# Kernel tuning notes

Measured on AMD Instinct MI355X. Metric: run time of the kernel, lower is better.

## Reference

```python
import jax, jax.numpy as jnp
import numpy as np

NUM_HEADS = 16


def setup_inputs() -> dict:
    key = jax.random.key(0)
    ks = jax.random.split(key, 6)
    B, S, E = 2, 2048, 1024
    scale = 1.0 / np.sqrt(E)
    return {
        "x": jax.random.normal(ks[0], (B, S, E), dtype=jnp.float32),
        "mask": jnp.ones((B, S), dtype=jnp.int32),
        "Wq": jax.random.normal(ks[1], (E, E), dtype=jnp.float32) * scale,
        "bq": jnp.zeros((E,), dtype=jnp.float32),
        "Wk": jax.random.normal(ks[2], (E, E), dtype=jnp.float32) * scale,
        "bk": jnp.zeros((E,), dtype=jnp.float32),
        "Wv": jax.random.normal(ks[3], (E, E), dtype=jnp.float32) * scale,
        "bv": jnp.zeros((E,), dtype=jnp.float32),
        "Wo": jax.random.normal(ks[4], (E, E), dtype=jnp.float32) * scale,
        "bo": jnp.zeros((E,), dtype=jnp.float32),
    }


def reference(x, mask, Wq, bq, Wk, bk, Wv, bv, Wo, bo):
    B, S, E = x.shape
    H = NUM_HEADS
    D = E // H

    def heads(t):  # [B,S,E] -> [B,H,S,D]
        return t.reshape(B, S, H, D).transpose(0, 2, 1, 3)

    q = heads(x @ Wq + bq)
    k = heads(x @ Wk + bk)
    v = heads(x @ Wv + bv)

    # scaled dot-product scores [B,H,S,S]
    scores = jnp.einsum("bhsd,bhtd->bhst", q, k) / jnp.sqrt(jnp.float32(D))
    m = mask.astype(jnp.float32)[:, None, None, :]  # key-side padding mask
    scores = scores + (-1e9) * (1.0 - m)
    weights = jax.nn.softmax(scores, axis=-1)
    attn = jnp.einsum("bhst,bhtd->bhsd", weights, v)

    concat = attn.transpose(0, 2, 1, 3).reshape(B, S, E)
    return concat @ Wo + bo
```

## Files before the change

kernel.cpp:

```cpp
#include <hip/hip_runtime.h>
#include <stdint.h>

#define E_DIM   1024
#define HNUM    16
#define DH      64
#define BATCH   2
#define SEQ     2048
#define M_TOT   (BATCH*SEQ)
#define LOG2E   1.44269504088896340736f

typedef __bf16 bf16x8 __attribute__((ext_vector_type(8)));
typedef __bf16 bf16x4 __attribute__((ext_vector_type(4)));
typedef float  f32x4  __attribute__((ext_vector_type(4)));
typedef float  f32x16 __attribute__((ext_vector_type(16)));
typedef unsigned short u16;
typedef unsigned int   u32;
typedef unsigned long long u64;
typedef u16 u16x8 __attribute__((ext_vector_type(8)));
typedef u32 u32x2 __attribute__((ext_vector_type(2)));
typedef u32 u32x4 __attribute__((ext_vector_type(4)));

__device__ __forceinline__ u16 f2bf(float f) {
    u32 u = __builtin_bit_cast(u32, f);
    u32 r = 0x7FFFu + ((u >> 16) & 1u);
    return (u16)((u + r) >> 16);
}

__device__ __forceinline__ void gload_lds16(const u16* g, u16* l) {
    __builtin_amdgcn_global_load_lds(
        (const __attribute__((address_space(1))) u32*)g,
        (__attribute__((address_space(3))) u32*)l, 16, 0, 0);
}

__device__ __forceinline__ u32 cvt_pk_bf16(float lo, float hi) {
    u32 r;
    asm("v_cvt_pk_bf16_f32 %0, %1, %2" : "=v"(r) : "v"(lo), "v"(hi));
    return r;
}

#define MFMA16(a,b,c) __builtin_amdgcn_mfma_f32_16x16x32_bf16((a),(b),(c),0,0,0)
#define MFMA32(a,b,c) __builtin_amdgcn_mfma_f32_32x32x16_bf16((a),(b),(c),0,0,0)

__global__ __launch_bounds__(256) void prep_kernel(
    const float* __restrict__ x, u16* __restrict__ out,
    const int* __restrict__ mask, u64* __restrict__ bits,
    const float* __restrict__ w0, const float* __restrict__ w1,
    const float* __restrict__ w2, const float* __restrict__ w3,
    u16* __restrict__ wt) {
    __shared__ float tile[32][33];
    const int bid = blockIdx.x;
    const int tid = threadIdx.x;
    if (bid < M_TOT * E_DIM / 1024) {
        const int idx = (bid * 256 + tid) * 4;
        float4 v = *reinterpret_cast<const float4*>(x + idx);
        ushort4 o;
        o.x = f2bf(v.x); o.y = f2bf(v.y); o.z = f2bf(v.z); o.w = f2bf(v.w);
        *reinterpret_cast<ushort4*>(out + idx) = o;
        if (bid < M_TOT / 256) {
            const int i = bid * 256 + tid;
            u64 bl = __ballot(mask[i] != 0);
            if ((i & 63) == 0) bits[i >> 6] = bl;
        }
    } else {
        const int wb = bid - M_TOT * E_DIM / 1024;
        const int z = wb >> 10;
        const int rem = wb & 1023;
        const int n0 = (rem & 31) * 32, k0 = (rem >> 5) * 32;
        const int tx = tid & 31, ty = tid >> 5;
        const float* w = z == 0 ? w0 : z == 1 ? w1 : z == 2 ? w2 : w3;
        #pragma unroll
        for (int j = 0; j < 4; j++) {
            int k = k0 + ty + j * 8;
            tile[ty + j * 8][tx] = w[(size_t)k * E_DIM + n0 + tx];
        }
        __syncthreads();
        u16* o = wt + (size_t)z * E_DIM * E_DIM;
        #pragma unroll
        for (int j = 0; j < 4; j++) {
            int n = n0 + ty + j * 8;
            o[(size_t)n * E_DIM + k0 + tx] = f2bf(tile[tx][ty + j * 8]);
        }
    }
}

template <typename OutT>
__global__ __launch_bounds__(256) void gemm_kernel(
    const u16* __restrict__ A, const u16* __restrict__ Bt_base, OutT* __restrict__ C_base,
    const float* __restrict__ bias0, const float* __restrict__ bias1,
    const float* __restrict__ bias2, float scale0, int Mdim) {
    const int z = blockIdx.z;
    const u16* Bt = Bt_base + (size_t)z * E_DIM * E_DIM;
    OutT* C = C_base + (size_t)z * Mdim * E_DIM;
    const float* bias = (z == 0) ? bias0 : (z == 1 ? bias1 : bias2);
    const float scale = (z == 0) ? scale0 : 1.0f;

    __shared__ __align__(16) u16 Als[128 * 32];
    __shared__ __align__(16) u16 Bls[128 * 32];

    const int tid = threadIdx.x;
    const int lane = tid & 63;
    const int w = tid >> 6;
    const int wr = (w >> 1) * 64, wc = (w & 1) * 64;
    const int tm = blockIdx.y * 128, tn = blockIdx.x * 128;
    const int r4 = tid >> 2;
    const int c8 = (tid & 3) * 8;

    f32x4 acc[4][4] = {};

    for (int k0 = 0; k0 < E_DIM; k0 += 32) {
        gload_lds16(A + (size_t)(tm + r4) * E_DIM + k0 + c8, Als + tid * 8);
        gload_lds16(A + (size_t)(tm + 64 + r4) * E_DIM + k0 + c8, Als + 2048 + tid * 8);
        gload_lds16(Bt + (size_t)(tn + r4) * E_DIM + k0 + c8, Bls + tid * 8);
        gload_lds16(Bt + (size_t)(tn + 64 + r4) * E_DIM + k0 + c8, Bls + 2048 + tid * 8);
        __syncthreads();
        const int lr = lane & 15, lg = lane >> 4;
        bf16x8 af[4], bfr[4];
        #pragma unroll
        for (int m = 0; m < 4; m++)
            af[m] = *reinterpret_cast<const bf16x8*>(Als + (wr + m * 16 + lr) * 32 + lg * 8);
        #pragma unroll
        for (int n = 0; n < 4; n++)
            bfr[n] = *reinterpret_cast<const bf16x8*>(Bls + (wc + n * 16 + lr) * 32 + lg * 8);
        #pragma unroll
        for (int m = 0; m < 4; m++)
            #pragma unroll
            for (int n = 0; n < 4; n++)
                acc[m][n] = MFMA16(af[m], bfr[n], acc[m][n]);
        __syncthreads();
    }

    const int lr = lane & 15, lg = lane >> 4;
    #pragma unroll
    for (int m = 0; m < 4; m++) {
        #pragma unroll
        for (int n = 0; n < 4; n++) {
            const int col = tn + wc + n * 16 + lr;
            const float bv = bias[col];
            #pragma unroll
            for (int r = 0; r < 4; r++) {
                const int row = tm + wr + m * 16 + lg * 4 + r;
                float v = (acc[m][n][r] + bv) * scale;
                if constexpr (sizeof(OutT) == 2) {
                    C[(size_t)row * E_DIM + col] = f2bf(v);
                } else {
                    C[(size_t)row * E_DIM + col] = v;
                }
            }
        }
    }
}

__global__ __launch_bounds__(512) void attn_kernel(
    const u16* __restrict__ Q, const u16* __restrict__ K, const u16* __restrict__ V,
    const u64* __restrict__ mbits, u16* __restrict__ PO, float* __restrict__ lws) {
    __shared__ __align__(16) u16 Kls[4][64 * 64];
    __shared__ __align__(16) u16 Vt[2][64 * 64];

    const int tid = threadIdx.x;
    const int lane = tid & 63;
    const int wave = tid >> 6;
    const int sub = wave >> 2;
    const int wg = wave & 3;
    const int hi = lane >> 5;
    const int l31 = lane & 31;
    const int n = blockIdx.x;
    const int g = n & 63, qt = n >> 6;
    const int h = g & 15, zz = g >> 4;
    const int b = zz >> 1, half = zz & 1;

    const int qrow = b * SEQ + qt * 256 + sub * 128 + wg * 32 + l31;
    bf16x8 qf[4];
    #pragma unroll
    for (int kc = 0; kc < 4; kc++)
        qf[kc] = *reinterpret_cast<const bf16x8*>(Q + (size_t)qrow * E_DIM + h * DH + kc * 16 + hi * 8);

    const int krow = (l31 & 3) | ((l31 & 4) << 1) | ((l31 & 8) >> 1) | (l31 & 16);
    const u32 ksw = (u32)(krow & 7) << 4;
    u32 koff[4];
    #pragma unroll
    for (int kc = 0; kc < 4; kc++)
        koff[kc] = (((u32)krow * 128) + (u32)kc * 32 + (u32)hi * 16) ^ ksw;

    const int krA = tid >> 3;
    const int kcA = (tid & 7) ^ (krA & 7);
    const size_t kgoff = (size_t)krA * E_DIM + kcA * 8;

    const int t8 = tid & 255;
    const int vhalf = tid >> 8;
    const int vc = t8 & 7;
    const int vsg = ((t8 >> 3) ^ (vc << 2)) & 31;
    const size_t vgoff = (size_t)(2 * vsg) * E_DIM + vc * 8 + vhalf * 4;
    u32 vwoff[4];
    #pragma unroll
    for (int jj = 0; jj < 4; jj++) {
        const int j = vhalf * 4 + jj;
        vwoff[jj] = (((u32)(vc * 8 + j) * 128) + (u32)vsg * 4) ^ ((u32)j << 4);
    }
    u32 vroff[4];
    #pragma unroll
    for (int kc = 0; kc < 4; kc++)
        vroff[kc] = (((u32)l31 * 128) + (u32)(2 * kc + hi) * 16) ^ (((u32)(l31 & 7)) << 4);

    f32x16 oacc0 = {}, oacc1 = {};
    f32x4 l4 = {};

    const u16* Kg = K + (size_t)(b * SEQ + half * (SEQ / 2)) * E_DIM + h * DH;
    const u16* Vg = V + (size_t)(b * SEQ + half * (SEQ / 2)) * E_DIM + h * DH;
    const size_t TSTEP = (size_t)64 * E_DIM;
    const u16* kgp = Kg + kgoff;
    const u16* vgp = Vg + vgoff;
    const int NT = SEQ / 2 / 64;

    {
        u32x2 a0 = *reinterpret_cast<const u32x2*>(vgp);
        u32x2 a1 = *reinterpret_cast<const u32x2*>(vgp + E_DIM);
        gload_lds16(kgp,             &Kls[0][tid * 8]);
        gload_lds16(kgp + TSTEP,     &Kls[1][tid * 8]);
        gload_lds16(kgp + 2 * TSTEP, &Kls[2][tid * 8]);
        kgp += 3 * TSTEP; vgp += TSTEP;
        asm volatile("s_waitcnt vmcnt(1)" ::: "memory");
        __builtin_amdgcn_sched_barrier(0);
        #pragma unroll
        for (int jj = 0; jj < 4; jj++)
            *(u32*)((char*)Vt + vwoff[jj]) = __builtin_amdgcn_perm(
                a1[jj >> 1], a0[jj >> 1], (jj & 1) ? 0x07060302u : 0x05040100u);
        asm volatile("s_waitcnt lgkmcnt(0)" ::: "memory");
        __builtin_amdgcn_sched_barrier(0);
        __builtin_amdgcn_s_barrier();
    }

    f32x16 sc0 = {}, sc1 = {}, sn0, sn1;
    {
        const char* Kb = (const char*)Kls;
        __builtin_amdgcn_s_setprio(1);
        #pragma unroll
        for (int kc = 0; kc < 4; kc++) {
            bf16x8 kf0 = *(const bf16x8*)(Kb + koff[kc]);
            bf16x8 kf1 = *(const bf16x8*)(Kb + koff[kc] + 4096);
            sc0 = MFMA32(kf0, qf[kc], sc0);
            sc1 = MFMA32(kf1, qf[kc], sc1);
        }
        __builtin_amdgcn_s_setprio(0);
    }

#define ATTN_TILE(T, CUR0, CUR1, NXT0, NXT1)                                           \
    {                                                                                  \
        const int t_ = (T);                                                            \
        const bool haveV = (t_ + 1 < NT);                                              \
        const bool haveK = (t_ + 3 < NT);                                              \
        u32x2 a0, a1;                                                                  \
        if (haveV) {                                                                   \
            a0 = *reinterpret_cast<const u32x2*>(vgp);                                 \
            a1 = *reinterpret_cast<const u32x2*>(vgp + E_DIM);                         \
        }                                                                              \
        if (haveK) gload_lds16(kgp, &Kls[(t_ + 3) & 3][tid * 8]);                      \
        const u64 mb = mbits[b * (SEQ / 64) + half * NT + t_];                         \
        if (mb != ~0ull) {                                                             \
            _Pragma("unroll")                                                          \
            for (int r = 0; r < 16; r++) {                                             \
                const int key = (r & 3) + 4 * ((r >> 2) & 1) + 8 * hi + 16 * ((r >> 3) & 1); \
                if (!((mb >> key) & 1))        CUR0[r] += -1.442695e9f;                \
                if (!((mb >> (32 + key)) & 1)) CUR1[r] += -1.442695e9f;                \
            }                                                                          \
        }                                                                              \
        _Pragma("unroll")                                                              \
        for (int r = 0; r < 16; r++) {                                                 \
            CUR0[r] = __builtin_amdgcn_exp2f(CUR0[r]); l4[r & 3] += CUR0[r];           \
        }                                                                              \
        _Pragma("unroll")                                                              \
        for (int r = 0; r < 16; r++) {                                                 \
            CUR1[r] = __builtin_amdgcn_exp2f(CUR1[r]); l4[r & 3] += CUR1[r];           \
        }                                                                              \
        bf16x8 pf[4];                                                                  \
        {                                                                              \
            u32x4 pw0, pw1, pw2, pw3;                                                  \
            _Pragma("unroll")                                                          \
            for (int e = 0; e < 4; e++) {                                              \
                pw0[e] = cvt_pk_bf16(CUR0[2 * e],     CUR0[2 * e + 1]);                \
                pw1[e] = cvt_pk_bf16(CUR0[8 + 2 * e], CUR0[9 + 2 * e]);                \
                pw2[e] = cvt_pk_bf16(CUR1[2 * e],     CUR1[2 * e + 1]);                \
                pw3[e] = cvt_pk_bf16(CUR1[8 + 2 * e], CUR1[9 + 2 * e]);                \
            }                                                                          \
            pf[0] = __builtin_bit_cast(bf16x8, pw0);                                   \
            pf[1] = __builtin_bit_cast(bf16x8, pw1);                                   \
            pf[2] = __builtin_bit_cast(bf16x8, pw2);                                   \
            pf[3] = __builtin_bit_cast(bf16x8, pw3);                                   \
        }                                                                              \
        NXT0 = f32x16{};                                                               \
        NXT1 = f32x16{};                                                               \
        if (haveV) {                                                                   \
            const char* Kb = (const char*)Kls + ((t_ + 1) & 3) * 8192;                 \
            __builtin_amdgcn_s_setprio(1);                                             \
            _Pragma("unroll")                                                          \
            for (int kc = 0; kc < 4; kc++) {                                           \
                bf16x8 kf0 = *(const bf16x8*)(Kb + koff[kc]);                          \
                bf16x8 kf1 = *(const bf16x8*)(Kb + koff[kc] + 4096);                   \
                NXT0 = MFMA32(kf0, qf[kc], NXT0);                                      \
                NXT1 = MFMA32(kf1, qf[kc], NXT1);                                      \
            }                                                                          \
            __builtin_amdgcn_s_setprio(0);                                             \
        }                                                                              \
        {                                                                              \
            const char* Vb = (const char*)Vt + (t_ & 1) * 8192;                        \
            __builtin_amdgcn_s_setprio(1);                                             \
            _Pragma("unroll")                                                          \
            for (int kc = 0; kc < 4; kc++) {                                           \
                bf16x8 vf0 = *(const bf16x8*)(Vb + vroff[kc]);                         \
                bf16x8 vf1 = *(const bf16x8*)(Vb + vroff[kc] + 4096);                  \
                oacc0 = MFMA32(vf0, pf[kc], oacc0);                                    \
                oacc1 = MFMA32(vf1, pf[kc], oacc1);                                    \
            }                                                                          \
            __builtin_amdgcn_s_setprio(0);                                             \
        }                                                                              \
        asm volatile("s_waitcnt vmcnt(1)" ::: "memory");                               \
        __builtin_amdgcn_sched_barrier(0);                                             \
        if (haveV) {                                                                   \
            _Pragma("unroll")                                                          \
            for (int jj = 0; jj < 4; jj++)                                             \
                *(u32*)((char*)Vt + ((t_ + 1) & 1) * 8192 + vwoff[jj]) =               \
                    __builtin_amdgcn_perm(a1[jj >> 1], a0[jj >> 1],                    \
                                          (jj & 1) ? 0x07060302u : 0x05040100u);       \
        }                                                                              \
        asm volatile("s_waitcnt lgkmcnt(0)" ::: "memory");                             \
        __builtin_amdgcn_sched_barrier(0);                                             \
        __builtin_amdgcn_s_barrier();                                                  \
        if (haveK) kgp += TSTEP;                                                       \
        if (haveV) vgp += TSTEP;                                                       \
    }

    for (int tp = 0; tp < NT / 2; tp++) {
        ATTN_TILE(2 * tp,     sc0, sc1, sn0, sn1)
        ATTN_TILE(2 * tp + 1, sn0, sn1, sc0, sc1)
    }
#undef ATTN_TILE

    const float l_run = (l4[0] + l4[1]) + (l4[2] + l4[3]);
    const float l_tot = l_run + __shfl_xor(l_run, 32);
    u16* op = PO + ((size_t)half * M_TOT + qrow) * E_DIM + h * DH;
    #pragma unroll
    for (int db = 0; db < 2; db++) {
        #pragma unroll
        for (int j = 0; j < 4; j++) {
            u32x2 pk;
            pk[0] = cvt_pk_bf16(db ? oacc1[4 * j + 0] : oacc0[4 * j + 0],
                                db ? oacc1[4 * j + 1] : oacc0[4 * j + 1]);
            pk[1] = cvt_pk_bf16(db ? oacc1[4 * j + 2] : oacc0[4 * j + 2],
                                db ? oacc1[4 * j + 3] : oacc0[4 * j + 3]);
            const int d0 = 32 * db + 8 * j + 4 * hi;
            *reinterpret_cast<u32x2*>(op + d0) = pk;
        }
    }
    if (hi == 0) lws[((size_t)half * M_TOT + qrow) * HNUM + h] = l_tot;
}

__global__ __launch_bounds__(256) void combine_kernel(const u16* __restrict__ PO,
                                                      const float* __restrict__ lws,
                                                      u16* __restrict__ ab) {
    const int i = (blockIdx.x * 256 + threadIdx.x) * 8;
    const int row = i >> 10;
    const int h = (i & 1023) >> 6;
    const float l0 = lws[(size_t)row * HNUM + h];
    const float l1 = lws[((size_t)M_TOT + row) * HNUM + h];
    const float rl = 1.0f / (l0 + l1);
    const bf16x8 a = *reinterpret_cast<const bf16x8*>(PO + i);
    const bf16x8 c = *reinterpret_cast<const bf16x8*>(PO + (size_t)M_TOT * E_DIM + i);
    u16x8 o;
    #pragma unroll
    for (int j = 0; j < 8; j++)
        o[j] = f2bf(((float)a[j] + (float)c[j]) * rl);
    *reinterpret_cast<u16x8*>(ab + i) = o;
}

extern "C" void kernel_launch(void* const* d_in, const int* in_sizes, int n_in,
                              void* d_out, int out_size, void* d_ws, size_t ws_size,
                              hipStream_t stream) {
    const float* x  = (const float*)d_in[0];
    const int* mask = (const int*)d_in[1];
    const float* Wq = (const float*)d_in[2];
    const float* bq = (const float*)d_in[3];
    const float* Wk = (const float*)d_in[4];
    const float* bk = (const float*)d_in[5];
    const float* Wv = (const float*)d_in[6];
    const float* bv = (const float*)d_in[7];
    const float* Wo = (const float*)d_in[8];
    const float* bo = (const float*)d_in[9];
    float* out = (float*)d_out;

    u16* ws  = (u16*)d_ws;
    const size_t ME = (size_t)M_TOT * E_DIM;
    u16* xb  = ws;
    u16* wt  = ws + ME;
    u16* qb  = ws + 2 * ME;
    u16* kbf = ws + 3 * ME;
    u16* vbf = ws + 4 * ME;
    u64* mbf = (u64*)(ws + 5 * ME);
    float* lws = (float*)(ws + 5 * ME + 8192);
    u16* ab  = xb;
    u16* po  = (u16*)d_out;

    prep_kernel<<<dim3(M_TOT * E_DIM / 1024 + 4096), dim3(256), 0, stream>>>(
        x, xb, mask, mbf, Wq, Wk, Wv, Wo, wt);
    gemm_kernel<u16><<<dim3(E_DIM / 128, M_TOT / 128, 3), dim3(256), 0, stream>>>(
        xb, wt, qb, bq, bk, bv, 0.125f * LOG2E, M_TOT);
    attn_kernel<<<dim3(512), dim3(512), 0, stream>>>(qb, kbf, vbf, mbf, po, lws);
    combine_kernel<<<dim3(M_TOT * E_DIM / 2048), dim3(256), 0, stream>>>(po, lws, ab);
    gemm_kernel<float><<<dim3(E_DIM / 128, M_TOT / 128, 1), dim3(256), 0, stream>>>(
        ab, wt + (size_t)3 * E_DIM * E_DIM, out, bo, bo, bo, 1.0f, M_TOT);
}
```

Baseline: 122.8 us.

## Fuse split-KV combine into attention kernel via last-arriver atomic ticket

Removes the separate combine kernel launch. Each attention block bumps a per-(head,batch,query-tile) counter after writing its partial output and row sums, and the second block to arrive merges both halves and writes the normalized bf16 activations. Flags are zeroed in the prep kernel. This saves a launch and a full-tensor pass, at the cost of a threadfence, an atomic, and a serialized tail on whichever block finishes last.

```diff
diff --git a/kernel.cpp b/kernel.cpp
--- a/kernel.cpp
+++ b/kernel.cpp
@@ -46,7 +46,7 @@
     const int* __restrict__ mask, u64* __restrict__ bits,
     const float* __restrict__ w0, const float* __restrict__ w1,
     const float* __restrict__ w2, const float* __restrict__ w3,
-    u16* __restrict__ wt) {
+    u16* __restrict__ wt, u32* __restrict__ flags) {
     __shared__ float tile[32][33];
     const int bid = blockIdx.x;
     const int tid = threadIdx.x;
@@ -61,6 +61,7 @@
             u64 bl = __ballot(mask[i] != 0);
             if ((i & 63) == 0) bits[i >> 6] = bl;
         }
+        if (bid == 0) flags[tid] = 0;
     } else {
         const int wb = bid - M_TOT * E_DIM / 1024;
         const int z = wb >> 10;
@@ -152,9 +153,11 @@
 
 __global__ __launch_bounds__(512) void attn_kernel(
     const u16* __restrict__ Q, const u16* __restrict__ K, const u16* __restrict__ V,
-    const u64* __restrict__ mbits, u16* __restrict__ PO, float* __restrict__ lws) {
+    const u64* __restrict__ mbits, u16* __restrict__ PO, float* __restrict__ lws,
+    u32* __restrict__ flags, u16* __restrict__ ab) {
     __shared__ __align__(16) u16 Kls[4][64 * 64];
     __shared__ __align__(16) u16 Vt[2][64 * 64];
+    __shared__ int ticket_old;
 
     const int tid = threadIdx.x;
     const int lane = tid & 63;
@@ -351,24 +354,33 @@
         }
     }
     if (hi == 0) lws[((size_t)half * M_TOT + qrow) * HNUM + h] = l_tot;
-}
-
-__global__ __launch_bounds__(256) void combine_kernel(const u16* __restrict__ PO,
-                                                      const float* __restrict__ lws,
-                                                      u16* __restrict__ ab) {
-    const int i = (blockIdx.x * 256 + threadIdx.x) * 8;
-    const int row = i >> 10;
-    const int h = (i & 1023) >> 6;
-    const float l0 = lws[(size_t)row * HNUM + h];
-    const float l1 = lws[((size_t)M_TOT + row) * HNUM + h];
-    const float rl = 1.0f / (l0 + l1);
-    const bf16x8 a = *reinterpret_cast<const bf16x8*>(PO + i);
-    const bf16x8 c = *reinterpret_cast<const bf16x8*>(PO + (size_t)M_TOT * E_DIM + i);
-    u16x8 o;
-    #pragma unroll
-    for (int j = 0; j < 8; j++)
-        o[j] = f2bf(((float)a[j] + (float)c[j]) * rl);
-    *reinterpret_cast<u16x8*>(ab + i) = o;
+
+    __threadfence();
+    __syncthreads();
+    if (tid == 0) ticket_old = (int)atomicAdd(&flags[h + 16 * b + 32 * qt], 1u);
+    __syncthreads();
+    if (ticket_old == 1) {
+        __threadfence();
+        const int rbase = b * SEQ + qt * 256;
+        #pragma unroll
+        for (int i = 0; i < 4; i++) {
+            const int c = tid + 512 * i;
+            const int row = rbase + (c >> 3);
+            const int col = h * DH + (c & 7) * 8;
+            const float l0 = lws[(size_t)row * HNUM + h];
+            const float l1 = lws[((size_t)M_TOT + row) * HNUM + h];
+            const float rl = 1.0f / (l0 + l1);
+            const bf16x8 pa = *reinterpret_cast<const bf16x8*>(
+                PO + (size_t)row * E_DIM + col);
+            const bf16x8 pb = *reinterpret_cast<const bf16x8*>(
+                PO + ((size_t)M_TOT + row) * E_DIM + col);
+            u16x8 o;
+            #pragma unroll
+            for (int j = 0; j < 8; j++)
+                o[j] = f2bf(((float)pa[j] + (float)pb[j]) * rl);
+            *reinterpret_cast<u16x8*>(ab + (size_t)row * E_DIM + col) = o;
+        }
+    }
 }
 
 extern "C" void kernel_launch(void* const* d_in, const int* in_sizes, int n_in,
@@ -395,15 +407,15 @@
     u16* vbf = ws + 4 * ME;
     u64* mbf = (u64*)(ws + 5 * ME);
     float* lws = (float*)(ws + 5 * ME + 8192);
+    u32* flags = (u32*)(ws + 5 * ME + 8192 + 262144);
     u16* ab  = xb;
     u16* po  = (u16*)d_out;
 
     prep_kernel<<<dim3(M_TOT * E_DIM / 1024 + 4096), dim3(256), 0, stream>>>(
-        x, xb, mask, mbf, Wq, Wk, Wv, Wo, wt);
+        x, xb, mask, mbf, Wq, Wk, Wv, Wo, wt, flags);
     gemm_kernel<u16><<<dim3(E_DIM / 128, M_TOT / 128, 3), dim3(256), 0, stream>>>(
         xb, wt, qb, bq, bk, bv, 0.125f * LOG2E, M_TOT);
-    attn_kernel<<<dim3(512), dim3(512), 0, stream>>>(qb, kbf, vbf, mbf, po, lws);
-    combine_kernel<<<dim3(M_TOT * E_DIM / 2048), dim3(256), 0, stream>>>(po, lws, ab);
+    attn_kernel<<<dim3(512), dim3(512), 0, stream>>>(qb, kbf, vbf, mbf, po, lws, flags, ab);
     gemm_kernel<float><<<dim3(E_DIM / 128, M_TOT / 128, 1), dim3(256), 0, stream>>>(
         ab, wt + (size_t)3 * E_DIM * E_DIM, out, bo, bo, bo, 1.0f, M_TOT);
 }
```

Result: slower. 314.4 us (+156.0%).
